# Performance work log

Hardware: AMD Instinct MI355X
Metric: run time of the kernel (lower is better)

Reference implementation:

```python
import jax, jax.numpy as jnp
from jax import lax
import numpy as np

I, H = 16, 32  # input_size, hidden_size
B, T = 8192, 512


def setup_inputs() -> dict:
    key = jax.random.key(0)
    ks = jax.random.split(key, 8)
    s_ih = 1.0 / np.sqrt(H)
    x = jax.random.normal(ks[0], (B, T, I), dtype=jnp.float32)
    # PyTorch LSTM params, gate order i,f,g,o along the 4H dim
    W_ih = jax.random.uniform(ks[1], (4 * H, I), minval=-s_ih, maxval=s_ih, dtype=jnp.float32)
    W_hh = jax.random.uniform(ks[2], (4 * H, H), minval=-s_ih, maxval=s_ih, dtype=jnp.float32)
    b_ih = jax.random.uniform(ks[3], (4 * H,), minval=-s_ih, maxval=s_ih, dtype=jnp.float32)
    b_hh = jax.random.uniform(ks[4], (4 * H,), minval=-s_ih, maxval=s_ih, dtype=jnp.float32)
    W_fc = jax.random.uniform(ks[5], (1, H), minval=-s_ih, maxval=s_ih, dtype=jnp.float32)
    b_fc = jax.random.uniform(ks[6], (1,), minval=-s_ih, maxval=s_ih, dtype=jnp.float32)
    return {"x": x, "W_ih": W_ih, "W_hh": W_hh, "b_ih": b_ih, "b_hh": b_hh,
            "W_fc": W_fc, "b_fc": b_fc}


def reference(x, W_ih, W_hh, b_ih, b_hh, W_fc, b_fc):
    # Precompute input contribution for all timesteps: [B, T, 4H]
    xg = jnp.einsum('bti,gi->btg', x, W_ih) + b_ih + b_hh

    def step(carry, g_t):  # g_t: [B, 4H]
        h, c = carry
        gates = g_t + h @ W_hh.T
        i, f, g, o = jnp.split(gates, 4, axis=-1)
        c = jax.nn.sigmoid(f) * c + jax.nn.sigmoid(i) * jnp.tanh(g)
        h = jax.nn.sigmoid(o) * jnp.tanh(c)
        return (h, c), None

    h0 = jnp.zeros((x.shape[0], H), dtype=x.dtype)
    (h_last, _), _ = lax.scan(step, (h0, h0), jnp.swapaxes(xg, 0, 1))
    # last_hidden -> dropout (eval mode: identity) -> fc -> squeeze
    out = h_last @ W_fc.T + b_fc  # [B, 1]
    return out.squeeze(-1)  # [B]
```

## Files before the change

### kernel.cpp

```cpp
#include <hip/hip_runtime.h>


typedef float f4 __attribute__((ext_vector_type(4)));
typedef __bf16 bf8v __attribute__((ext_vector_type(8)));

constexpr int ISZ = 16, HSZ = 32, TT = 512, BB = 8192;
constexpr int HSTR = 72;
constexpr int XSTR = 40;

#define MFMA32(a, b, c) __builtin_amdgcn_mfma_f32_16x16x32_bf16((a), (b), (c), 0, 0, 0)

__device__ __forceinline__ float fsig(float x) {
  return __builtin_amdgcn_rcpf(1.0f + __builtin_amdgcn_exp2f(-1.44269504f * x));
}

__device__ __forceinline__ void split8(const float* v, bf8v& hi, bf8v& lo) {
#pragma unroll
  for (int i = 0; i < 8; ++i) {
    const __bf16 h = (__bf16)v[i];
    hi[i] = h;
    lo[i] = (__bf16)(v[i] - (float)h);
  }
}

__global__ __launch_bounds__(512, 4) void lstm_mfma(
    const float* __restrict__ x, const float* __restrict__ W_ih,
    const float* __restrict__ W_hh, const float* __restrict__ b_ih,
    const float* __restrict__ b_hh, const float* __restrict__ W_fc,
    const float* __restrict__ b_fc, float* __restrict__ out) {
  __shared__ __align__(16) __bf16 hl[2][16][HSTR];
  __shared__ __align__(16) __bf16 xs[2][16][XSTR];
  __shared__ __align__(16) float gbuf[4][16][HSZ + 1];

  const int tid = threadIdx.x;
  const int wv = tid >> 6;
  const int g = wv & 3;
  const int uh = wv >> 2;
  const int L = tid & 63;
  const int m = L & 15;
  const int q = L >> 4;
  const int row0 = blockIdx.x * 16;
  const int uw = uh * 16 + m;
  const int j = g * 32 + uw;

  const int eR = wv * 2 + (L >> 5);
  const int eu = L & 31;

  bf8v bih1, bih2, bhh1, bhh2;
  f4 biasv;
  {
    float wh[8];
    *(f4*)&wh[0] = *(const f4*)(W_hh + j * HSZ + 8 * q);
    *(f4*)&wh[4] = *(const f4*)(W_hh + j * HSZ + 8 * q + 4);
    split8(wh, bhh1, bhh2);
    float wi[8];
    const int k8 = (q & 1) * 8;
    *(f4*)&wi[0] = *(const f4*)(W_ih + j * ISZ + k8);
    *(f4*)&wi[4] = *(const f4*)(W_ih + j * ISZ + k8 + 4);
    split8(wi, bih1, bih2);
    const float bb = b_ih[j] + b_hh[j];
    biasv = (f4){bb, bb, bb, bb};
  }

  for (int i = tid; i < 2 * 16 * HSTR; i += 512) ((__bf16*)hl)[i] = (__bf16)0.0f;
  const int xr = tid >> 4, xi = tid & 15;
  const float* xbase = x + (size_t)(row0 + xr) * TT * ISZ + xi;
  if (tid < 256) {
    const float v = xbase[0];
    const __bf16 h = (__bf16)v;
    xs[0][xr][xi] = h;
    xs[0][xr][16 + xi] = (__bf16)(v - (float)h);
  }
  __syncthreads();

  float cst = 0.0f;

  for (int t = 0; t < TT; ++t) {
    const int p = t & 1;
    const bf8v ax  = *(const bf8v*)&xs[p][m][8 * q];
    const bf8v ah1 = *(const bf8v*)&hl[p][m][8 * q];
    const bf8v ah2 = *(const bf8v*)&hl[p][m][32 + 8 * q];

    float xnext = 0.0f;
    const int tn = (t < TT - 1) ? t + 1 : t;
    if (tid < 256) xnext = xbase[(size_t)tn * ISZ];

    f4 a = MFMA32(ax, bih1, biasv);
    a = MFMA32(ax, bih2, a);
    a = MFMA32(ah1, bhh1, a);
    a = MFMA32(ah2, bhh1, a);
    a = MFMA32(ah1, bhh2, a);

#pragma unroll
    for (int r = 0; r < 4; ++r) gbuf[g][q * 4 + r][uw] = a[r];
    __syncthreads();

    const float vi = gbuf[0][eR][eu];
    const float vf = gbuf[1][eR][eu];
    const float vg = gbuf[2][eR][eu];
    const float vo = gbuf[3][eR][eu];

    const float ig = fsig(vi);
    const float fg = fsig(vf);
    const float gv = 2.0f * fsig(2.0f * vg) - 1.0f;
    const float og = fsig(vo);
    const float cc = fg * cst + ig * gv;
    cst = cc;
    const float th = 2.0f * fsig(2.0f * cc) - 1.0f;
    const float h = og * th;
    const __bf16 h1 = (__bf16)h;
    hl[p ^ 1][eR][eu] = h1;
    hl[p ^ 1][eR][32 + eu] = (__bf16)(h - (float)h1);

    if (tid < 256) {
      const __bf16 xh = (__bf16)xnext;
      xs[p ^ 1][xr][xi] = xh;
      xs[p ^ 1][xr][16 + xi] = (__bf16)(xnext - (float)xh);
    }
    __syncthreads();
  }

  if (tid < 16) {
    float s = b_fc[0];
#pragma unroll 8
    for (int uu = 0; uu < HSZ; ++uu) {
      const float h = (float)hl[0][tid][uu] + (float)hl[0][tid][32 + uu];
      s += h * W_fc[uu];
    }
    out[row0 + tid] = s;
  }
}

extern "C" void kernel_launch(void* const* d_in, const int* in_sizes, int n_in,
                              void* d_out, int out_size, void* d_ws, size_t ws_size,
                              hipStream_t stream) {
  const float* x    = (const float*)d_in[0];
  const float* W_ih = (const float*)d_in[1];
  const float* W_hh = (const float*)d_in[2];
  const float* b_ih = (const float*)d_in[3];
  const float* b_hh = (const float*)d_in[4];
  const float* W_fc = (const float*)d_in[5];
  const float* b_fc = (const float*)d_in[6];
  float* out = (float*)d_out;

  dim3 grid(BB / 16);
  dim3 block(512);
  lstm_mfma<<<grid, block, 0, stream>>>(x, W_ih, W_hh, b_ih, b_hh, W_fc, b_fc, out);
}
```

Measured before the change: 629.4 us.

## Make each wavefront an independent LSTM over 8 rows, removing block barriers

Each 64-lane wavefront now owns 8 batch rows and computes all four gates for both unit halves from register-resident split-bf16 weights. Gate activations are done straight from the MFMA accumulators, and h goes through per-wave LDS, so the per-step __syncthreads and the gate-exchange buffer are gone. x is loaded directly into registers and split on the fly. The cost is duplicated MFMA rows, which doubles the MFMA work per row. It also brings very high register pressure and only one 256-thread block per CU, so there is less latency hiding across the serial time loop.

```diff
diff --git a/kernel.cpp b/kernel.cpp
--- a/kernel.cpp
+++ b/kernel.cpp
@@ -5,8 +5,9 @@
 typedef __bf16 bf8v __attribute__((ext_vector_type(8)));
 
 constexpr int ISZ = 16, HSZ = 32, TT = 512, BB = 8192;
-constexpr int HSTR = 72;
-constexpr int XSTR = 40;
+constexpr int RPW = 8;
+constexpr int WPB = 4;
+constexpr int HST = 40;
 
 #define MFMA32(a, b, c) __builtin_amdgcn_mfma_f32_16x16x32_bf16((a), (b), (c), 0, 0, 0)
 
@@ -23,111 +24,118 @@
   }
 }
 
-__global__ __launch_bounds__(512, 4) void lstm_mfma(
+__global__ __launch_bounds__(256, 1) void lstm_mfma(
     const float* __restrict__ x, const float* __restrict__ W_ih,
     const float* __restrict__ W_hh, const float* __restrict__ b_ih,
     const float* __restrict__ b_hh, const float* __restrict__ W_fc,
     const float* __restrict__ b_fc, float* __restrict__ out) {
-  __shared__ __align__(16) __bf16 hl[2][16][HSTR];
-  __shared__ __align__(16) __bf16 xs[2][16][XSTR];
-  __shared__ __align__(16) float gbuf[4][16][HSZ + 1];
+  __shared__ __align__(16) __bf16 hlds[WPB][2][2][RPW][HST];
 
   const int tid = threadIdx.x;
   const int wv = tid >> 6;
-  const int g = wv & 3;
-  const int uh = wv >> 2;
   const int L = tid & 63;
   const int m = L & 15;
   const int q = L >> 4;
-  const int row0 = blockIdx.x * 16;
-  const int uw = uh * 16 + m;
-  const int j = g * 32 + uw;
+  const int mr = m & 7;
+  const int qr = q & 1;
+  const int qh = q >> 1;
+  const int u_own = qh * 16 + m;
+  const int row0 = (blockIdx.x * WPB + wv) * RPW;
 
-  const int eR = wv * 2 + (L >> 5);
-  const int eu = L & 31;
+  bf8v wih1[4][2], wih2[4][2], whh1[4][2], whh2[4][2];
+  float bb[4][2];
+#pragma unroll
+  for (int g = 0; g < 4; ++g)
+#pragma unroll
+    for (int uh = 0; uh < 2; ++uh) {
+      const int j = g * 32 + uh * 16 + m;
+      float wh[8];
+      *(f4*)&wh[0] = *(const f4*)(W_hh + j * HSZ + 8 * q);
+      *(f4*)&wh[4] = *(const f4*)(W_hh + j * HSZ + 8 * q + 4);
+      split8(wh, whh1[g][uh], whh2[g][uh]);
+      float wi[8];
+      *(f4*)&wi[0] = *(const f4*)(W_ih + j * ISZ + 8 * qr);
+      *(f4*)&wi[4] = *(const f4*)(W_ih + j * ISZ + 8 * qr + 4);
+      split8(wi, wih1[g][uh], wih2[g][uh]);
+      bb[g][uh] = b_ih[j] + b_hh[j];
+    }
 
-  bf8v bih1, bih2, bhh1, bhh2;
-  f4 biasv;
   {
-    float wh[8];
-    *(f4*)&wh[0] = *(const f4*)(W_hh + j * HSZ + 8 * q);
-    *(f4*)&wh[4] = *(const f4*)(W_hh + j * HSZ + 8 * q + 4);
-    split8(wh, bhh1, bhh2);
-    float wi[8];
-    const int k8 = (q & 1) * 8;
-    *(f4*)&wi[0] = *(const f4*)(W_ih + j * ISZ + k8);
-    *(f4*)&wi[4] = *(const f4*)(W_ih + j * ISZ + k8 + 4);
-    split8(wi, bih1, bih2);
-    const float bb = b_ih[j] + b_hh[j];
-    biasv = (f4){bb, bb, bb, bb};
+    __bf16* z = &hlds[wv][0][0][0][0];
+    for (int i = L; i < 2 * RPW * HST; i += 64) z[i] = (__bf16)0.0f;
   }
 
-  for (int i = tid; i < 2 * 16 * HSTR; i += 512) ((__bf16*)hl)[i] = (__bf16)0.0f;
-  const int xr = tid >> 4, xi = tid & 15;
-  const float* xbase = x + (size_t)(row0 + xr) * TT * ISZ + xi;
-  if (tid < 256) {
-    const float v = xbase[0];
-    const __bf16 h = (__bf16)v;
-    xs[0][xr][xi] = h;
-    xs[0][xr][16 + xi] = (__bf16)(v - (float)h);
-  }
-  __syncthreads();
+  const float* xrp = x + (size_t)(row0 + mr) * TT * ISZ + 8 * qr;
+  f4 xc0 = *(const f4*)(xrp);
+  f4 xc1 = *(const f4*)(xrp + 4);
 
-  float cst = 0.0f;
+  float cst[4] = {0.0f, 0.0f, 0.0f, 0.0f};
 
   for (int t = 0; t < TT; ++t) {
     const int p = t & 1;
-    const bf8v ax  = *(const bf8v*)&xs[p][m][8 * q];
-    const bf8v ah1 = *(const bf8v*)&hl[p][m][8 * q];
-    const bf8v ah2 = *(const bf8v*)&hl[p][m][32 + 8 * q];
+    const bf8v ah1 = *(const bf8v*)&hlds[wv][p][0][mr][8 * q];
+    const bf8v ah2 = *(const bf8v*)&hlds[wv][p][1][mr][8 * q];
 
-    float xnext = 0.0f;
     const int tn = (t < TT - 1) ? t + 1 : t;
-    if (tid < 256) xnext = xbase[(size_t)tn * ISZ];
+    const f4 xn0 = *(const f4*)(xrp + (size_t)tn * ISZ);
+    const f4 xn1 = *(const f4*)(xrp + (size_t)tn * ISZ + 4);
 
-    f4 a = MFMA32(ax, bih1, biasv);
-    a = MFMA32(ax, bih2, a);
-    a = MFMA32(ah1, bhh1, a);
-    a = MFMA32(ah2, bhh1, a);
-    a = MFMA32(ah1, bhh2, a);
+    bf8v ax;
+#pragma unroll
+    for (int jj = 0; jj < 8; ++jj) {
+      const float v = (jj < 4) ? xc0[jj] : xc1[jj - 4];
+      const __bf16 hi = (__bf16)v;
+      const __bf16 lo = (__bf16)(v - (float)hi);
+      ax[jj] = (q < 2) ? hi : lo;
+    }
 
+    f4 acc[4][2];
 #pragma unroll
-    for (int r = 0; r < 4; ++r) gbuf[g][q * 4 + r][uw] = a[r];
-    __syncthreads();
+    for (int g = 0; g < 4; ++g)
+#pragma unroll
+      for (int uh = 0; uh < 2; ++uh) {
+        const f4 c = (f4){bb[g][uh], bb[g][uh], bb[g][uh], bb[g][uh]};
+        f4 a = MFMA32(ax, wih1[g][uh], c);
+        a = MFMA32(ax, wih2[g][uh], a);
+        a = MFMA32(ah1, whh1[g][uh], a);
+        a = MFMA32(ah2, whh1[g][uh], a);
+        a = MFMA32(ah1, whh2[g][uh], a);
+        acc[g][uh] = a;
+      }
+    xc0 = xn0;
+    xc1 = xn1;
 
-    const float vi = gbuf[0][eR][eu];
-    const float vf = gbuf[1][eR][eu];
-    const float vg = gbuf[2][eR][eu];
-    const float vo = gbuf[3][eR][eu];
-
-    const float ig = fsig(vi);
-    const float fg = fsig(vf);
-    const float gv = 2.0f * fsig(2.0f * vg) - 1.0f;
-    const float og = fsig(vo);
-    const float cc = fg * cst + ig * gv;
-    cst = cc;
-    const float th = 2.0f * fsig(2.0f * cc) - 1.0f;
-    const float h = og * th;
-    const __bf16 h1 = (__bf16)h;
-    hl[p ^ 1][eR][eu] = h1;
-    hl[p ^ 1][eR][32 + eu] = (__bf16)(h - (float)h1);
-
-    if (tid < 256) {
-      const __bf16 xh = (__bf16)xnext;
-      xs[p ^ 1][xr][xi] = xh;
-      xs[p ^ 1][xr][16 + xi] = (__bf16)(xnext - (float)xh);
+    const bool hiQ = (q >= 2);
+#pragma unroll
+    for (int r = 0; r < 4; ++r) {
+      const float vi = hiQ ? acc[0][1][r] : acc[0][0][r];
+      const float vf = hiQ ? acc[1][1][r] : acc[1][0][r];
+      const float vg = hiQ ? acc[2][1][r] : acc[2][0][r];
+      const float vo = hiQ ? acc[3][1][r] : acc[3][0][r];
+      const float ig = fsig(vi);
+      const float fg = fsig(vf);
+      const float gv = 2.0f * fsig(2.0f * vg) - 1.0f;
+      const float og = fsig(vo);
+      const float cc = fg * cst[r] + ig * gv;
+      cst[r] = cc;
+      const float th = 2.0f * fsig(2.0f * cc) - 1.0f;
+      const float h = og * th;
+      const __bf16 h1 = (__bf16)h;
+      const int row = 4 * qr + r;
+      hlds[wv][p ^ 1][0][row][u_own] = h1;
+      hlds[wv][p ^ 1][1][row][u_own] = (__bf16)(h - (float)h1);
     }
-    __syncthreads();
   }
 
-  if (tid < 16) {
+  if (L < RPW) {
     float s = b_fc[0];
 #pragma unroll 8
     for (int uu = 0; uu < HSZ; ++uu) {
-      const float h = (float)hl[0][tid][uu] + (float)hl[0][tid][32 + uu];
+      const float h =
+          (float)hlds[wv][0][0][L][uu] + (float)hlds[wv][0][1][L][uu];
       s += h * W_fc[uu];
     }
-    out[row0 + tid] = s;
+    out[row0 + L] = s;
   }
 }
 
@@ -143,7 +151,7 @@
   const float* b_fc = (const float*)d_in[6];
   float* out = (float*)d_out;
 
-  dim3 grid(BB / 16);
-  dim3 block(512);
+  dim3 grid(BB / (RPW * WPB));
+  dim3 block(64 * WPB);
   lstm_mfma<<<grid, block, 0, stream>>>(x, W_ih, W_hh, b_ih, b_hh, W_fc, b_fc, out);
 }
```

Measured after the change: 702.5 us. +11.6%, slower.
